# Kernel optimization log

Hardware: AMD Instinct MI355X
Metric: run time of the kernel (lower is better)

The kernel has to match this reference:

```python
import jax, jax.numpy as jnp
import numpy as np

S = 100  # spatial_encoding_size

def setup_inputs() -> dict:
    key = jax.random.key(0)
    k1, k2 = jax.random.split(key)
    N, C, B = 1000000, 64, 32
    agent_encodings = jax.random.normal(k1, (N, C), dtype=jnp.float32)
    encode_coordinates = jax.random.randint(k2, (N,), 0, B * S * S, dtype=jnp.int64)
    return {"batch_size": B, "agent_encodings": agent_encodings, "encode_coordinates": encode_coordinates}

def reference(batch_size, agent_encodings, encode_coordinates):
    N, C = agent_encodings.shape
    num_seg = batch_size * S * S
    # max over all agents mapped to each flat grid cell (-inf for empty cells)
    seg_max = jax.ops.segment_max(agent_encodings, encode_coordinates, num_segments=num_seg)
    counts = jax.ops.segment_sum(jnp.ones((N,), dtype=agent_encodings.dtype), encode_coordinates, num_segments=num_seg)
    occupied = counts > 0
    grid = jnp.where(occupied[:, None], seg_max, jnp.zeros((), dtype=agent_encodings.dtype))
    grid = grid.reshape(batch_size, S, S, C)
    return jnp.transpose(grid, (0, 3, 1, 2))  # [B, C, S, S]
```

## Files before the change

### kernel.cpp

```cpp
#include <hip/hip_runtime.h>
#include <math.h>


#define S_DIM 100
#define CELLS_PER_B (S_DIM * S_DIM)
#define C_DIM 64
#define CPB 32

__global__ void init_head(int* __restrict__ head, int n) {
    const int stride = gridDim.x * blockDim.x;
    for (int i = blockIdx.x * blockDim.x + threadIdx.x; i < n; i += stride)
        head[i] = -1;
}

__global__ void build_lists(const int* __restrict__ coords,
                            int* __restrict__ head, int* __restrict__ next,
                            int n) {
    const int stride = gridDim.x * blockDim.x;
    for (int i = blockIdx.x * blockDim.x + threadIdx.x; i < n; i += stride) {
        const int c = coords[i];
        next[i] = atomicExch(&head[c], i);
    }
}

__global__ __launch_bounds__(512) void gather_max(
    const float* __restrict__ enc, const int* __restrict__ head,
    const int* __restrict__ next, float* __restrict__ out) {
    __shared__ float tile[CPB][C_DIM + 1];
    const int tid = threadIdx.x;
    const int cl = tid >> 4;
    const int c4 = (tid & 15) << 2;
    const int b = blockIdx.y;
    const int rem0 = blockIdx.x * CPB;
    const int rem = rem0 + cl;

    float4 m = make_float4(-INFINITY, -INFINITY, -INFINITY, -INFINITY);
    int agent = (rem < CELLS_PER_B) ? head[b * CELLS_PER_B + rem] : -1;
    const bool occupied = (agent >= 0);
    while (agent >= 0) {
        const int nxt = next[agent];
        const float4 v =
            *reinterpret_cast<const float4*>(enc + (size_t)agent * C_DIM + c4);
        m.x = fmaxf(m.x, v.x);
        m.y = fmaxf(m.y, v.y);
        m.z = fmaxf(m.z, v.z);
        m.w = fmaxf(m.w, v.w);
        agent = nxt;
    }
    if (!occupied) m = make_float4(0.f, 0.f, 0.f, 0.f);
    tile[cl][c4 + 0] = m.x;
    tile[cl][c4 + 1] = m.y;
    tile[cl][c4 + 2] = m.z;
    tile[cl][c4 + 3] = m.w;
    __syncthreads();

    float* base = out + ((size_t)b * C_DIM) * CELLS_PER_B + rem0;
    const int limit = min(CPB, CELLS_PER_B - rem0);
    for (int i = tid; i < CPB * C_DIM; i += 512) {
        const int c = i >> 5;
        const int j = i & 31;
        if (j < limit) base[(size_t)c * CELLS_PER_B + j] = tile[j][c];
    }
}

extern "C" void kernel_launch(void* const* d_in, const int* in_sizes, int n_in,
                              void* d_out, int out_size, void* d_ws, size_t ws_size,
                              hipStream_t stream) {
    const float* enc = (const float*)d_in[1];
    const int* coords = (const int*)d_in[2];
    const int n = in_sizes[2];
    const int ncells = out_size / C_DIM;
    const int B = ncells / CELLS_PER_B;

    int* head = (int*)d_ws;
    int* next = head + ncells;

    init_head<<<1024, 256, 0, stream>>>(head, ncells);
    build_lists<<<2048, 256, 0, stream>>>(coords, head, next, n);
    dim3 grid((CELLS_PER_B + CPB - 1) / CPB, B);
    gather_max<<<grid, 512, 0, stream>>>(enc, head, next, (float*)d_out);
}
```

Before: 132.5 us.

## Replace per-cell linked lists with CSR bucketing via count, scan, and fill

Builds a CSR layout of agent indices per grid cell: atomic counts, a two-level exclusive scan, then an atomic fill of an order array. The gather kernel then reads contiguous index ranges instead of chasing next pointers. This removes the serial dependent loads of the linked-list traversal and allows unrolled, independent loads. The cost is several extra kernel launches, an extra pass over coords with atomics, and a single-block carry scan. The old linked-list path remains as a fallback when the workspace is too small.

```diff
diff --git a/kernel.cpp b/kernel.cpp
--- a/kernel.cpp
+++ b/kernel.cpp
@@ -7,12 +7,133 @@
 #define C_DIM 64
 #define CPB 32
 
+
+__global__ void init_counts(int* __restrict__ cnt, int n) {
+    const int stride = gridDim.x * blockDim.x;
+    for (int i = blockIdx.x * blockDim.x + threadIdx.x; i < n; i += stride)
+        cnt[i] = 0;
+}
+
+__global__ void count_agents(const int* __restrict__ coords,
+                             int* __restrict__ cnt, int n) {
+    const int stride = gridDim.x * blockDim.x;
+    for (int i = blockIdx.x * blockDim.x + threadIdx.x; i < n; i += stride)
+        atomicAdd(&cnt[coords[i]], 1);
+}
+
+__global__ void scan_blocks(const int* __restrict__ cnt, int* __restrict__ offs,
+                            int* __restrict__ bsum, int n) {
+    __shared__ int s[256];
+    const int t = threadIdx.x;
+    const int idx = blockIdx.x * 256 + t;
+    const int v = (idx < n) ? cnt[idx] : 0;
+    s[t] = v;
+    __syncthreads();
+    for (int off = 1; off < 256; off <<= 1) {
+        int x = (t >= off) ? s[t - off] : 0;
+        __syncthreads();
+        s[t] += x;
+        __syncthreads();
+    }
+    if (idx < n) offs[idx] = s[t] - v;
+    if (t == 255) bsum[blockIdx.x] = s[255];
+}
+
+__global__ void scan_carry(int* __restrict__ bsum, int nb) {
+    __shared__ int s[256];
+    __shared__ int carry;
+    const int t = threadIdx.x;
+    if (t == 0) carry = 0;
+    __syncthreads();
+    for (int base = 0; base < nb; base += 256) {
+        const int v = (base + t < nb) ? bsum[base + t] : 0;
+        s[t] = v;
+        __syncthreads();
+        for (int off = 1; off < 256; off <<= 1) {
+            int x = (t >= off) ? s[t - off] : 0;
+            __syncthreads();
+            s[t] += x;
+            __syncthreads();
+        }
+        const int tot = s[255];
+        const int ex = carry + s[t] - v;
+        if (base + t < nb) bsum[base + t] = ex;
+        __syncthreads();
+        if (t == 0) carry += tot;
+        __syncthreads();
+    }
+}
+
+__global__ void finalize_offs(int* __restrict__ offs, int* __restrict__ wptr,
+                              const int* __restrict__ bsum, int n) {
+    const int stride = gridDim.x * blockDim.x;
+    for (int i = blockIdx.x * blockDim.x + threadIdx.x; i < n; i += stride) {
+        const int o = offs[i] + bsum[i >> 8];
+        offs[i] = o;
+        wptr[i] = o;
+    }
+}
+
+__global__ void fill_order(const int* __restrict__ coords,
+                           int* __restrict__ wptr, int* __restrict__ order,
+                           int n) {
+    const int stride = gridDim.x * blockDim.x;
+    for (int i = blockIdx.x * blockDim.x + threadIdx.x; i < n; i += stride) {
+        const int pos = atomicAdd(&wptr[coords[i]], 1);
+        order[pos] = i;
+    }
+}
+
+__global__ __launch_bounds__(512) void gather_csr(
+    const float* __restrict__ enc, const int* __restrict__ offs,
+    const int* __restrict__ cnt, const int* __restrict__ order,
+    float* __restrict__ out) {
+    __shared__ float tile[CPB][C_DIM + 1];
+    const int tid = threadIdx.x;
+    const int cl = tid >> 4;
+    const int c4 = (tid & 15) << 2;
+    const int b = blockIdx.y;
+    const int rem0 = blockIdx.x * CPB;
+    const int rem = rem0 + cl;
+
+    int start = 0, L = 0;
+    if (rem < CELLS_PER_B) {
+        const int cell = b * CELLS_PER_B + rem;
+        start = offs[cell];
+        L = cnt[cell];
+    }
+    float4 m = make_float4(-INFINITY, -INFINITY, -INFINITY, -INFINITY);
+#pragma unroll 4
+    for (int i = 0; i < L; ++i) {
+        const int a = order[start + i];
+        const float4 v =
+            *reinterpret_cast<const float4*>(enc + (size_t)a * C_DIM + c4);
+        m.x = fmaxf(m.x, v.x);
+        m.y = fmaxf(m.y, v.y);
+        m.z = fmaxf(m.z, v.z);
+        m.w = fmaxf(m.w, v.w);
+    }
+    if (L == 0) m = make_float4(0.f, 0.f, 0.f, 0.f);
+    tile[cl][c4 + 0] = m.x;
+    tile[cl][c4 + 1] = m.y;
+    tile[cl][c4 + 2] = m.z;
+    tile[cl][c4 + 3] = m.w;
+    __syncthreads();
+
+    float* base = out + ((size_t)b * C_DIM) * CELLS_PER_B + rem0;
+    const int limit = min(CPB, CELLS_PER_B - rem0);
+    for (int i = tid; i < CPB * C_DIM; i += 512) {
+        const int c = i >> 5;
+        const int j = i & 31;
+        if (j < limit) base[(size_t)c * CELLS_PER_B + j] = tile[j][c];
+    }
+}
+
 __global__ void init_head(int* __restrict__ head, int n) {
     const int stride = gridDim.x * blockDim.x;
     for (int i = blockIdx.x * blockDim.x + threadIdx.x; i < n; i += stride)
         head[i] = -1;
 }
-
 __global__ void build_lists(const int* __restrict__ coords,
                             int* __restrict__ head, int* __restrict__ next,
                             int n) {
@@ -22,8 +143,7 @@
         next[i] = atomicExch(&head[c], i);
     }
 }
-
-__global__ __launch_bounds__(512) void gather_max(
+__global__ __launch_bounds__(512) void gather_ll(
     const float* __restrict__ enc, const int* __restrict__ head,
     const int* __restrict__ next, float* __restrict__ out) {
     __shared__ float tile[CPB][C_DIM + 1];
@@ -53,7 +173,6 @@
     tile[cl][c4 + 2] = m.z;
     tile[cl][c4 + 3] = m.w;
     __syncthreads();
-
     float* base = out + ((size_t)b * C_DIM) * CELLS_PER_B + rem0;
     const int limit = min(CPB, CELLS_PER_B - rem0);
     for (int i = tid; i < CPB * C_DIM; i += 512) {
@@ -71,12 +190,32 @@
     const int n = in_sizes[2];
     const int ncells = out_size / C_DIM;
     const int B = ncells / CELLS_PER_B;
-
-    int* head = (int*)d_ws;
-    int* next = head + ncells;
-
-    init_head<<<1024, 256, 0, stream>>>(head, ncells);
-    build_lists<<<2048, 256, 0, stream>>>(coords, head, next, n);
-    dim3 grid((CELLS_PER_B + CPB - 1) / CPB, B);
-    gather_max<<<grid, 512, 0, stream>>>(enc, head, next, (float*)d_out);
-}
+    const int nb = (ncells + 255) / 256;
+
+    const size_t need_csr =
+        ((size_t)3 * ncells + (size_t)n + (size_t)nb) * sizeof(int);
+    dim3 ggrid((CELLS_PER_B + CPB - 1) / CPB, B);
+
+    if (ws_size >= need_csr) {
+        int* cnt = (int*)d_ws;
+        int* offs = cnt + ncells;
+        int* wptr = offs + ncells;
+        int* order = wptr + ncells;
+        int* bsum = order + n;
+
+        init_counts<<<512, 256, 0, stream>>>(cnt, ncells);
+        count_agents<<<2048, 256, 0, stream>>>(coords, cnt, n);
+        scan_blocks<<<nb, 256, 0, stream>>>(cnt, offs, bsum, ncells);
+        scan_carry<<<1, 256, 0, stream>>>(bsum, nb);
+        finalize_offs<<<512, 256, 0, stream>>>(offs, wptr, bsum, ncells);
+        fill_order<<<2048, 256, 0, stream>>>(coords, wptr, order, n);
+        gather_csr<<<ggrid, 512, 0, stream>>>(enc, offs, cnt, order,
+                                              (float*)d_out);
+    } else {
+        int* head = (int*)d_ws;
+        int* next = head + ncells;
+        init_head<<<512, 256, 0, stream>>>(head, ncells);
+        build_lists<<<2048, 256, 0, stream>>>(coords, head, next, n);
+        gather_ll<<<ggrid, 512, 0, stream>>>(enc, head, next, (float*)d_out);
+    }
+}
```

New measurement: 217.1 us. 1.64x slower.

## Use wave-per-cell gather, vectorized list build, and atomic-max fallback path

Applied to the files above, without the earlier changes.

The gather kernel now gives each 64-lane wave one cell at a time and walks that cell's agent list with scalar per-lane loads. Previously 16 threads handled a cell using float4 loads, which made lanes in a wave follow different list lengths. List building now reads coordinates as int4 and stores the next pointers as int4, which cuts the number of memory instructions. The launch grids are halved. A fallback path for when the workspace is too small scatters values with encoded atomicMax into the output and then decodes it, adding a second code path that the default workspace normally does not use.

```diff
diff --git a/kernel.cpp b/kernel.cpp
--- a/kernel.cpp
+++ b/kernel.cpp
@@ -16,42 +16,51 @@
 __global__ void build_lists(const int* __restrict__ coords,
                             int* __restrict__ head, int* __restrict__ next,
                             int n) {
+    const int n4 = n >> 2;
     const int stride = gridDim.x * blockDim.x;
-    for (int i = blockIdx.x * blockDim.x + threadIdx.x; i < n; i += stride) {
-        const int c = coords[i];
-        next[i] = atomicExch(&head[c], i);
+    const int4* c4p = reinterpret_cast<const int4*>(coords);
+    for (int i = blockIdx.x * blockDim.x + threadIdx.x; i < n4; i += stride) {
+        const int4 c = c4p[i];
+        const int base = i << 2;
+        int4 nx;
+        nx.x = atomicExch(&head[c.x], base + 0);
+        nx.y = atomicExch(&head[c.y], base + 1);
+        nx.z = atomicExch(&head[c.z], base + 2);
+        nx.w = atomicExch(&head[c.w], base + 3);
+        reinterpret_cast<int4*>(next)[i] = nx;
+    }
+    const int tail0 = n4 << 2;
+    const int gtid = blockIdx.x * blockDim.x + threadIdx.x;
+    if (gtid < n - tail0) {
+        const int i = tail0 + gtid;
+        next[i] = atomicExch(&head[coords[i]], i);
     }
 }
 
-__global__ __launch_bounds__(512) void gather_max(
+__global__ __launch_bounds__(512) void gather_ll(
     const float* __restrict__ enc, const int* __restrict__ head,
     const int* __restrict__ next, float* __restrict__ out) {
     __shared__ float tile[CPB][C_DIM + 1];
     const int tid = threadIdx.x;
-    const int cl = tid >> 4;
-    const int c4 = (tid & 15) << 2;
+    const int lane = tid & 63;
+    const int wave = tid >> 6;
     const int b = blockIdx.y;
     const int rem0 = blockIdx.x * CPB;
-    const int rem = rem0 + cl;
 
-    float4 m = make_float4(-INFINITY, -INFINITY, -INFINITY, -INFINITY);
-    int agent = (rem < CELLS_PER_B) ? head[b * CELLS_PER_B + rem] : -1;
-    const bool occupied = (agent >= 0);
-    while (agent >= 0) {
-        const int nxt = next[agent];
-        const float4 v =
-            *reinterpret_cast<const float4*>(enc + (size_t)agent * C_DIM + c4);
-        m.x = fmaxf(m.x, v.x);
-        m.y = fmaxf(m.y, v.y);
-        m.z = fmaxf(m.z, v.z);
-        m.w = fmaxf(m.w, v.w);
-        agent = nxt;
+#pragma unroll
+    for (int k = 0; k < CPB / 8; ++k) {
+        const int cl = wave + (k << 3);
+        const int rem = rem0 + cl;
+        float m = -INFINITY;
+        int agent = (rem < CELLS_PER_B) ? head[b * CELLS_PER_B + rem] : -1;
+        const bool occupied = (agent >= 0);
+        while (agent >= 0) {
+            const int nxt = next[agent];
+            m = fmaxf(m, enc[(size_t)agent * C_DIM + lane]);
+            agent = nxt;
+        }
+        tile[cl][lane] = occupied ? m : 0.f;
     }
-    if (!occupied) m = make_float4(0.f, 0.f, 0.f, 0.f);
-    tile[cl][c4 + 0] = m.x;
-    tile[cl][c4 + 1] = m.y;
-    tile[cl][c4 + 2] = m.z;
-    tile[cl][c4 + 3] = m.w;
     __syncthreads();
 
     float* base = out + ((size_t)b * C_DIM) * CELLS_PER_B + rem0;
@@ -60,6 +69,50 @@
         const int c = i >> 5;
         const int j = i & 31;
         if (j < limit) base[(size_t)c * CELLS_PER_B + j] = tile[j][c];
+    }
+}
+
+__device__ __forceinline__ unsigned encode_f32(float f) {
+    unsigned u = __float_as_uint(f);
+    return (u & 0x80000000u) ? ~u : (u | 0x80000000u);
+}
+__device__ __forceinline__ float decode_key(unsigned k) {
+    if (k == 0u) return 0.0f;
+    return (k & 0x80000000u) ? __uint_as_float(k & 0x7FFFFFFFu)
+                             : __uint_as_float(~k);
+}
+__global__ void spatial_scatter_max(const float* __restrict__ enc,
+                                    const int* __restrict__ coords,
+                                    unsigned* __restrict__ grid, int n_agents) {
+    const long long total = (long long)n_agents * 16;
+    const long long stride = (long long)gridDim.x * blockDim.x;
+    for (long long i = (long long)blockIdx.x * blockDim.x + threadIdx.x;
+         i < total; i += stride) {
+        const int agent = (int)(i >> 4);
+        const int c4 = ((int)i & 15) << 2;
+        const int coord = coords[agent];
+        const int b = coord / CELLS_PER_B;
+        const int rem = coord - b * CELLS_PER_B;
+        const float4 v =
+            *reinterpret_cast<const float4*>(enc + (size_t)agent * C_DIM + c4);
+        unsigned* p = grid + ((size_t)b * C_DIM + c4) * CELLS_PER_B + rem;
+        atomicMax(p, encode_f32(v.x));
+        atomicMax(p + 1 * CELLS_PER_B, encode_f32(v.y));
+        atomicMax(p + 2 * CELLS_PER_B, encode_f32(v.z));
+        atomicMax(p + 3 * CELLS_PER_B, encode_f32(v.w));
+    }
+}
+__global__ void spatial_decode(unsigned* __restrict__ grid, int n4) {
+    const int stride = gridDim.x * blockDim.x;
+    uint4* g4 = reinterpret_cast<uint4*>(grid);
+    for (int i = blockIdx.x * blockDim.x + threadIdx.x; i < n4; i += stride) {
+        uint4 k = g4[i];
+        float4 f;
+        f.x = decode_key(k.x);
+        f.y = decode_key(k.y);
+        f.z = decode_key(k.z);
+        f.w = decode_key(k.w);
+        reinterpret_cast<float4*>(g4)[i] = f;
     }
 }
 
@@ -72,11 +125,18 @@
     const int ncells = out_size / C_DIM;
     const int B = ncells / CELLS_PER_B;
 
-    int* head = (int*)d_ws;
-    int* next = head + ncells;
-
-    init_head<<<1024, 256, 0, stream>>>(head, ncells);
-    build_lists<<<2048, 256, 0, stream>>>(coords, head, next, n);
-    dim3 grid((CELLS_PER_B + CPB - 1) / CPB, B);
-    gather_max<<<grid, 512, 0, stream>>>(enc, head, next, (float*)d_out);
+    const size_t need = ((size_t)ncells + (size_t)n) * sizeof(int);
+    if (ws_size >= need) {
+        int* head = (int*)d_ws;
+        int* next = head + ncells;
+        init_head<<<512, 256, 0, stream>>>(head, ncells);
+        build_lists<<<1024, 256, 0, stream>>>(coords, head, next, n);
+        dim3 grid((CELLS_PER_B + CPB - 1) / CPB, B);
+        gather_ll<<<grid, 512, 0, stream>>>(enc, head, next, (float*)d_out);
+    } else {
+        unsigned* out = (unsigned*)d_out;
+        hipMemsetAsync(d_out, 0, (size_t)out_size * sizeof(float), stream);
+        spatial_scatter_max<<<2048, 256, 0, stream>>>(enc, coords, out, n);
+        spatial_decode<<<2048, 256, 0, stream>>>(out, out_size / 4);
+    }
 }
```

Result: slower. 187.9 us (+41.9%).
